# Performance work log

Hardware: AMD Instinct MI355X
Metric: run time of the kernel (lower is better)

## Reference

```python
import jax, jax.numpy as jnp
import numpy as np

B, T, D, R = 4, 2048, 1024, 32


def setup_inputs() -> dict:
    key = jax.random.key(0)
    kx, ku = jax.random.split(key)
    x = jax.random.normal(kx, (B, T, D), dtype=jnp.float32)
    # low-rank metric factor; small init so distances are moderate
    U = jax.random.normal(ku, (D, R), dtype=jnp.float32) * 0.05
    return {"x": x, "U": U}


def reference(x, U):
    # g = U @ U.T (PSD low-rank metric).
    # dist_sq[b,t,j] = (x_t - x_j)^T g (x_t - x_j)
    #               = ||U^T x_t||^2 + ||U^T x_j||^2 - 2 (U^T x_t).(U^T x_j)
    # Algebraic expansion of the original O(B*T*T*D) broadcasted diff tensor.
    y = jnp.einsum('btd,dr->btr', x, U)                # [B,T,R]
    n = jnp.sum(y * y, axis=-1)                         # [B,T]
    cross = jnp.einsum('btr,bjr->btj', y, y)            # [B,T,T]
    dist_sq = n[:, :, None] + n[:, None, :] - 2.0 * cross
    attn = jax.nn.softmax(-dist_sq, axis=-1)            # [B,T,T]
    return jnp.einsum('btj,bjd->btd', attn, x)          # [B,T,D]
```

## Files before the change

### kernel.cpp

```cpp
#include <hip/hip_runtime.h>

#define B_ 4
#define T_ 2048
#define D_ 1024
#define R_ 32
#define XSTR2 136
#define TT 64
#define TD 128
#define TJ 64
#define PSTR 72

typedef __attribute__((ext_vector_type(8))) short short8;
typedef __attribute__((ext_vector_type(4))) float f32x4;
typedef __attribute__((ext_vector_type(4))) unsigned short us4;
typedef __attribute__((ext_vector_type(8))) unsigned short us8;

__device__ __forceinline__ unsigned short f2bf(float f) {
  union { float f; unsigned u; } v; v.f = f;
  unsigned r = (v.u + 0x7fffu + ((v.u >> 16) & 1u)) >> 16;
  return (unsigned short)r;
}
__device__ __forceinline__ float bf2f(unsigned short h) {
  union { unsigned u; float f; } v; v.u = (unsigned)h << 16;
  return v.f;
}

__global__ __launch_bounds__(256)
void geo_ut(const float* __restrict__ U, unsigned short* __restrict__ Ut) {
  __shared__ float tile[128][33];
  const int tid = threadIdx.x;
  const int d0 = blockIdx.x * 128;
  #pragma unroll
  for (int i = 0; i < 16; i++) {
    int e = i * 256 + tid;
    int d = e >> 5, r = e & 31;
    tile[d][r] = U[(size_t)(d0 + d) * R_ + r];
  }
  __syncthreads();
  const int r = tid >> 3, seg = tid & 7;
  us8 o0, o1;
  #pragma unroll
  for (int k = 0; k < 8; k++) o0[k] = f2bf(tile[seg * 16 + k][r]);
  #pragma unroll
  for (int k = 0; k < 8; k++) o1[k] = f2bf(tile[seg * 16 + 8 + k][r]);
  *(us8*)(Ut + (size_t)r * D_ + d0 + seg * 16) = o0;
  *(us8*)(Ut + (size_t)r * D_ + d0 + seg * 16 + 8) = o1;
}

__global__ __launch_bounds__(256)
void geo_prep(const float* __restrict__ x, const unsigned short* __restrict__ Ut,
              unsigned short* __restrict__ xt, float* __restrict__ y_part) {
  __shared__ unsigned short xs[2][32 * XSTR2];
  const int b = blockIdx.y, slab = blockIdx.z;
  const int t0 = blockIdx.x * 32;
  const int d0 = slab * 256;
  const int tid = threadIdx.x, w = tid >> 6, lane = tid & 63;
  const int m = lane & 15, quad = lane >> 4;
  const int Mt = w & 1, Nt = w >> 1;
  const int lr = tid >> 3;
  const int lc = (tid & 7) * 16;

  const float* xb = x + ((size_t)b * T_ + t0 + lr) * D_ + d0 + lc;
  float4 v[2][4];
  #pragma unroll
  for (int ch = 0; ch < 2; ch++)
    #pragma unroll
    for (int i = 0; i < 4; i++)
      v[ch][i] = *(const float4*)(xb + ch * 128 + i * 4);
  #pragma unroll
  for (int ch = 0; ch < 2; ch++)
    #pragma unroll
    for (int i = 0; i < 4; i++) {
      us4 c;
      c[0] = f2bf(v[ch][i].x); c[1] = f2bf(v[ch][i].y);
      c[2] = f2bf(v[ch][i].z); c[3] = f2bf(v[ch][i].w);
      *(us4*)&xs[ch][lr * XSTR2 + lc + i * 4] = c;
    }
  __syncthreads();
  {
    const int wd = tid >> 1, wt = (tid & 1) * 16;
    #pragma unroll
    for (int ch = 0; ch < 2; ch++) {
      us8 o0, o1;
      #pragma unroll
      for (int k = 0; k < 8; k++) {
        o0[k] = xs[ch][(wt + k) * XSTR2 + wd];
        o1[k] = xs[ch][(wt + 8 + k) * XSTR2 + wd];
      }
      unsigned short* xo = xt + ((size_t)b * D_ + d0 + ch * 128 + wd) * T_ + t0;
      *(us8*)(xo + wt) = o0;
      *(us8*)(xo + wt + 8) = o1;
    }
  }
  f32x4 acc = {0.f, 0.f, 0.f, 0.f};
  #pragma unroll
  for (int ch = 0; ch < 2; ch++)
    #pragma unroll
    for (int ks = 0; ks < 4; ks++) {
      short8 af = *(const short8*)&xs[ch][(Mt * 16 + m) * XSTR2 + ks * 32 + quad * 8];
      short8 bf = *(const short8*)(Ut + (size_t)(Nt * 16 + m) * D_ + d0 + ch * 128 + ks * 32 + quad * 8);
      acc = __builtin_amdgcn_mfma_f32_16x16x32_bf16(af, bf, acc, 0, 0, 0);
    }
  float* yp = y_part + ((size_t)(slab * B_ + b) * T_ + t0 + Mt * 16 + quad * 4) * R_ + Nt * 16 + m;
  #pragma unroll
  for (int k = 0; k < 4; k++) yp[(size_t)k * R_] = acc[k];
}

__global__ __launch_bounds__(256)
void geo_reduce(const float* __restrict__ y_part, unsigned short* __restrict__ ybf,
                float* __restrict__ nsq) {
  const int tid = threadIdx.x;
  const size_t row = (size_t)blockIdx.x * 32 + (tid >> 3);
  const int r0 = (tid & 7) * 4;
  f32x4 v = {0.f, 0.f, 0.f, 0.f};
  #pragma unroll
  for (int s = 0; s < 4; s++) {
    f32x4 p = *(const f32x4*)(y_part + ((size_t)s * B_ * T_ + row) * R_ + r0);
    #pragma unroll
    for (int k = 0; k < 4; k++) v[k] += p[k];
  }
  us4 pk;
  float part = 0.f;
  #pragma unroll
  for (int k = 0; k < 4; k++) {
    pk[k] = f2bf(1.41421356237f * v[k]);
    float b = bf2f(pk[k]);
    part += b * b;
  }
  *(us4*)(ybf + row * R_ + r0) = pk;
  part += __shfl_xor(part, 1, 64);
  part += __shfl_xor(part, 2, 64);
  part += __shfl_xor(part, 4, 64);
  if ((tid & 7) == 0) nsq[row] = 0.5f * part;
}

__global__ __launch_bounds__(256)
void geo_fused(const unsigned short* __restrict__ ybf,
               const float* __restrict__ nsq,
               const unsigned short* __restrict__ xt,
               float* __restrict__ out) {
  __shared__ unsigned short XtS[TD * TJ];
  __shared__ unsigned short Pbuf[TT * PSTR];
  __shared__ float lred[4][TT];
  const int b = blockIdx.z;
  const int dt = blockIdx.x & 7, tt = blockIdx.x >> 3;
  const int t0 = tt * TT, d0 = dt * TD;
  const int tid = threadIdx.x, w = tid >> 6, lane = tid & 63;
  const int m = lane & 15, quad = lane >> 4;
  const int srow = lane >> 3, sslot = lane & 7;
  const unsigned short* yb = ybf + (size_t)b * T_ * R_;
  const float* nb = nsq + (size_t)b * T_;
  const unsigned short* xtb = xt + ((size_t)b * D_ + d0) * T_;

  short8 aq[4]; f32x4 ntv[4];
  #pragma unroll
  for (int s = 0; s < 4; s++) {
    aq[s]  = *(const short8*)(yb + (size_t)(t0 + s * 16 + m) * R_ + quad * 8);
    ntv[s] = *(const f32x4*)(nb + t0 + s * 16 + quad * 4);
  }
  f32x4 acc[4][2];
  f32x4 lsum[4];
  #pragma unroll
  for (int s = 0; s < 4; s++) {
    lsum[s] = (f32x4){0.f, 0.f, 0.f, 0.f};
    acc[s][0] = (f32x4){0.f, 0.f, 0.f, 0.f};
    acc[s][1] = (f32x4){0.f, 0.f, 0.f, 0.f};
  }

  for (int j0 = 0; j0 < T_; j0 += TJ) {
    if (j0) __syncthreads();
    #pragma unroll
    for (int cc = 0; cc < 4; cc++) {
      const int rd = w * 32 + cc * 8 + srow;
      const int gs = sslot ^ (rd & 7);
      __builtin_amdgcn_global_load_lds(
          (const __attribute__((address_space(1))) void*)(xtb + (size_t)rd * T_ + j0 + gs * 8),
          (__attribute__((address_space(3))) void*)(XtS + (w * 32 + cc * 8) * 64),
          16, 0, 0);
    }
    short8 bj = *(const short8*)(yb + (size_t)(j0 + w * 16 + m) * R_ + quad * 8);
    float nj = nb[j0 + w * 16 + m];
    #pragma unroll
    for (int s = 0; s < 4; s++) {
      f32x4 z = {0.f, 0.f, 0.f, 0.f};
      f32x4 c = __builtin_amdgcn_mfma_f32_16x16x32_bf16(aq[s], bj, z, 0, 0, 0);
      #pragma unroll
      for (int r = 0; r < 4; r++) {
        float p = __expf(c[r] - nj - ntv[s][r]);
        lsum[s][r] += p;
        Pbuf[(s * 16 + quad * 4 + r) * PSTR + w * 16 + m] = f2bf(p);
      }
    }
    __syncthreads();
    short8 bx[2][2];
    #pragma unroll
    for (int nt = 0; nt < 2; nt++) {
      const int dloc = w * 32 + nt * 16 + m;
      #pragma unroll
      for (int ks = 0; ks < 2; ks++)
        bx[nt][ks] = *(const short8*)(XtS + dloc * 64 + (((ks * 4 + quad) ^ (m & 7)) * 8));
    }
    #pragma unroll
    for (int s = 0; s < 4; s++) {
      short8 a0 = *(const short8*)(Pbuf + (s * 16 + m) * PSTR + quad * 8);
      short8 a1 = *(const short8*)(Pbuf + (s * 16 + m) * PSTR + 32 + quad * 8);
      #pragma unroll
      for (int nt = 0; nt < 2; nt++) {
        acc[s][nt] = __builtin_amdgcn_mfma_f32_16x16x32_bf16(a0, bx[nt][0], acc[s][nt], 0, 0, 0);
        acc[s][nt] = __builtin_amdgcn_mfma_f32_16x16x32_bf16(a1, bx[nt][1], acc[s][nt], 0, 0, 0);
      }
    }
  }
  #pragma unroll
  for (int s = 0; s < 4; s++)
    #pragma unroll
    for (int r = 0; r < 4; r++) {
      float v = lsum[s][r];
      v += __shfl_xor(v, 1, 64);
      v += __shfl_xor(v, 2, 64);
      v += __shfl_xor(v, 4, 64);
      v += __shfl_xor(v, 8, 64);
      lsum[s][r] = v;
    }
  if (m == 0) {
    #pragma unroll
    for (int s = 0; s < 4; s++)
      *(f32x4*)&lred[w][s * 16 + quad * 4] = lsum[s];
  }
  __syncthreads();
  float* ob = out + ((size_t)b * T_ + t0) * D_ + d0;
  #pragma unroll
  for (int s = 0; s < 4; s++) {
    f32x4 lt = *(const f32x4*)&lred[0][s * 16 + quad * 4];
    #pragma unroll
    for (int ww = 1; ww < 4; ww++) {
      f32x4 lv = *(const f32x4*)&lred[ww][s * 16 + quad * 4];
      #pragma unroll
      for (int r = 0; r < 4; r++) lt[r] += lv[r];
    }
    f32x4 inv;
    #pragma unroll
    for (int r = 0; r < 4; r++) inv[r] = 1.f / lt[r];
    #pragma unroll
    for (int nt = 0; nt < 2; nt++)
      #pragma unroll
      for (int r = 0; r < 4; r++)
        ob[(size_t)(s * 16 + quad * 4 + r) * D_ + w * 32 + nt * 16 + m] =
            acc[s][nt][r] * inv[r];
  }
}

extern "C" void kernel_launch(void* const* d_in, const int* in_sizes, int n_in,
                              void* d_out, int out_size, void* d_ws, size_t ws_size,
                              hipStream_t stream) {
  const float* x = (const float*)d_in[0];
  const float* U = (const float*)d_in[1];
  float* out = (float*)d_out;

  const size_t xt_b  = (size_t)B_ * D_ * T_ * 2;
  const size_t ybf_b = (size_t)B_ * T_ * R_ * 2;
  const size_t nsq_b = (size_t)B_ * T_ * 4;
  const size_t ut_b  = (size_t)D_ * R_ * 2;
  const size_t yp_b  = (size_t)4 * B_ * T_ * R_ * 4;

  char* wp = (char*)d_ws;
  unsigned short* xtp = (unsigned short*)wp;           wp += xt_b;
  unsigned short* ybf = (unsigned short*)wp;           wp += ybf_b;
  float* nsq = (float*)wp;                             wp += nsq_b;
  unsigned short* Utp = (unsigned short*)wp;           wp += ut_b;
  float* ypart = (float*)wp;                           wp += yp_b;
  (void)ws_size;

  hipLaunchKernelGGL(geo_ut, dim3(D_ / 128), dim3(256), 0, stream, U, Utp);
  hipLaunchKernelGGL(geo_prep, dim3(T_ / 32, B_, 4), dim3(256), 0, stream,
                     x, Utp, xtp, ypart);
  hipLaunchKernelGGL(geo_reduce, dim3(B_ * T_ / 32), dim3(256), 0, stream,
                     ypart, ybf, nsq);
  hipLaunchKernelGGL(geo_fused, dim3((T_ / TT) * (D_ / TD), 1, B_), dim3(256), 0, stream,
                     ybf, nsq, xtp, out);
}
```

Baseline: 181.8 us.

## Widen D tile to 256, use exp2 with folded log2e, transpose score MFMA

The feature tile per block doubles from 128 to 256 columns. The distance MFMA and the exponentials for each (t, j) tile are therefore computed half as often across the D dimension, and each wave now accumulates four 16-column output sub-tiles. The log2(e) factor is folded into the y scaling so the softmax can use exp2 directly. The score MFMA operands are swapped so each lane writes a contiguous us4 into the probability buffer and the row sum needs fewer shuffles. In exchange the grid has half as many blocks per batch and more accumulator registers are live, which may hurt occupancy. The launch-grid size must also match the new tile mapping, and that code is not shown.

New measurement: 158.6 us. 12.8% less time.

```diff
diff --git a/kernel.cpp b/kernel.cpp
--- a/kernel.cpp
+++ b/kernel.cpp
@@ -6,9 +6,10 @@
 #define R_ 32
 #define XSTR2 136
 #define TT 64
-#define TD 128
+#define TD 256
 #define TJ 64
 #define PSTR 72
+#define S2L 1.6986436f
 
 typedef __attribute__((ext_vector_type(8))) short short8;
 typedef __attribute__((ext_vector_type(4))) float f32x4;
@@ -123,7 +124,7 @@
   float part = 0.f;
   #pragma unroll
   for (int k = 0; k < 4; k++) {
-    pk[k] = f2bf(1.41421356237f * v[k]);
+    pk[k] = f2bf(S2L * v[k]);
     float b = bf2f(pk[k]);
     part += b * b;
   }
@@ -143,7 +144,7 @@
   __shared__ unsigned short Pbuf[TT * PSTR];
   __shared__ float lred[4][TT];
   const int b = blockIdx.z;
-  const int dt = blockIdx.x & 7, tt = blockIdx.x >> 3;
+  const int dt = blockIdx.x & 3, tt = blockIdx.x >> 2;
   const int t0 = tt * TT, d0 = dt * TD;
   const int tid = threadIdx.x, w = tid >> 6, lane = tid & 63;
   const int m = lane & 15, quad = lane >> 4;
@@ -152,80 +153,78 @@
   const float* nb = nsq + (size_t)b * T_;
   const unsigned short* xtb = xt + ((size_t)b * D_ + d0) * T_;
 
-  short8 aq[4]; f32x4 ntv[4];
-  #pragma unroll
-  for (int s = 0; s < 4; s++) {
-    aq[s]  = *(const short8*)(yb + (size_t)(t0 + s * 16 + m) * R_ + quad * 8);
-    ntv[s] = *(const f32x4*)(nb + t0 + s * 16 + quad * 4);
-  }
-  f32x4 acc[4][2];
-  f32x4 lsum[4];
-  #pragma unroll
-  for (int s = 0; s < 4; s++) {
-    lsum[s] = (f32x4){0.f, 0.f, 0.f, 0.f};
-    acc[s][0] = (f32x4){0.f, 0.f, 0.f, 0.f};
-    acc[s][1] = (f32x4){0.f, 0.f, 0.f, 0.f};
-  }
+  short8 bt[4]; float ntv[4];
+  #pragma unroll
+  for (int s = 0; s < 4; s++) {
+    bt[s]  = *(const short8*)(yb + (size_t)(t0 + s * 16 + m) * R_ + quad * 8);
+    ntv[s] = nb[t0 + s * 16 + m];
+  }
+  f32x4 acc[4][4];
+  float lsum[4] = {0.f, 0.f, 0.f, 0.f};
+  #pragma unroll
+  for (int s = 0; s < 4; s++)
+    #pragma unroll
+    for (int nt = 0; nt < 4; nt++)
+      acc[s][nt] = (f32x4){0.f, 0.f, 0.f, 0.f};
 
   for (int j0 = 0; j0 < T_; j0 += TJ) {
     if (j0) __syncthreads();
     #pragma unroll
-    for (int cc = 0; cc < 4; cc++) {
-      const int rd = w * 32 + cc * 8 + srow;
+    for (int cc = 0; cc < 8; cc++) {
+      const int rd = w * 64 + cc * 8 + srow;
       const int gs = sslot ^ (rd & 7);
       __builtin_amdgcn_global_load_lds(
           (const __attribute__((address_space(1))) void*)(xtb + (size_t)rd * T_ + j0 + gs * 8),
-          (__attribute__((address_space(3))) void*)(XtS + (w * 32 + cc * 8) * 64),
+          (__attribute__((address_space(3))) void*)(XtS + (w * 64 + cc * 8) * 64),
           16, 0, 0);
     }
-    short8 bj = *(const short8*)(yb + (size_t)(j0 + w * 16 + m) * R_ + quad * 8);
-    float nj = nb[j0 + w * 16 + m];
+    short8 aj = *(const short8*)(yb + (size_t)(j0 + w * 16 + m) * R_ + quad * 8);
+    f32x4 njv = *(const f32x4*)(nb + j0 + w * 16 + quad * 4);
     #pragma unroll
     for (int s = 0; s < 4; s++) {
       f32x4 z = {0.f, 0.f, 0.f, 0.f};
-      f32x4 c = __builtin_amdgcn_mfma_f32_16x16x32_bf16(aq[s], bj, z, 0, 0, 0);
+      f32x4 c = __builtin_amdgcn_mfma_f32_16x16x32_bf16(aj, bt[s], z, 0, 0, 0);
+      us4 pk;
+      float ls = 0.f;
       #pragma unroll
       for (int r = 0; r < 4; r++) {
-        float p = __expf(c[r] - nj - ntv[s][r]);
-        lsum[s][r] += p;
-        Pbuf[(s * 16 + quad * 4 + r) * PSTR + w * 16 + m] = f2bf(p);
+        float p = __builtin_exp2f(c[r] - njv[r] - ntv[s]);
+        ls += p;
+        pk[r] = f2bf(p);
       }
+      lsum[s] += ls;
+      *(us4*)(Pbuf + (s * 16 + m) * PSTR + w * 16 + quad * 4) = pk;
     }
     __syncthreads();
-    short8 bx[2][2];
-    #pragma unroll
-    for (int nt = 0; nt < 2; nt++) {
-      const int dloc = w * 32 + nt * 16 + m;
+    short8 bx[4][2];
+    #pragma unroll
+    for (int nt = 0; nt < 4; nt++) {
+      const int dloc = w * 64 + nt * 16 + m;
       #pragma unroll
       for (int ks = 0; ks < 2; ks++)
-        bx[nt][ks] = *(const short8*)(XtS + dloc * 64 + (((ks * 4 + quad) ^ (m & 7)) * 8));
+        bx[nt][ks] = *(const short8*)(XtS + dloc * 64 + (((ks * 4 + quad) ^ (dloc & 7)) * 8));
     }
     #pragma unroll
     for (int s = 0; s < 4; s++) {
       short8 a0 = *(const short8*)(Pbuf + (s * 16 + m) * PSTR + quad * 8);
       short8 a1 = *(const short8*)(Pbuf + (s * 16 + m) * PSTR + 32 + quad * 8);
       #pragma unroll
-      for (int nt = 0; nt < 2; nt++) {
+      for (int nt = 0; nt < 4; nt++) {
         acc[s][nt] = __builtin_amdgcn_mfma_f32_16x16x32_bf16(a0, bx[nt][0], acc[s][nt], 0, 0, 0);
         acc[s][nt] = __builtin_amdgcn_mfma_f32_16x16x32_bf16(a1, bx[nt][1], acc[s][nt], 0, 0, 0);
       }
     }
   }
   #pragma unroll
-  for (int s = 0; s < 4; s++)
-    #pragma unroll
-    for (int r = 0; r < 4; r++) {
-      float v = lsum[s][r];
-      v += __shfl_xor(v, 1, 64);
-      v += __shfl_xor(v, 2, 64);
-      v += __shfl_xor(v, 4, 64);
-      v += __shfl_xor(v, 8, 64);
-      lsum[s][r] = v;
-    }
-  if (m == 0) {
-    #pragma unroll
-    for (int s = 0; s < 4; s++)
-      *(f32x4*)&lred[w][s * 16 + quad * 4] = lsum[s];
+  for (int s = 0; s < 4; s++) {
+    float v = lsum[s];
+    v += __shfl_xor(v, 16, 64);
+    v += __shfl_xor(v, 32, 64);
+    lsum[s] = v;
+  }
+  if (quad == 0) {
+    #pragma unroll
+    for (int s = 0; s < 4; s++) lred[w][s * 16 + m] = lsum[s];
   }
   __syncthreads();
   float* ob = out + ((size_t)b * T_ + t0) * D_ + d0;
@@ -242,10 +241,10 @@
     #pragma unroll
     for (int r = 0; r < 4; r++) inv[r] = 1.f / lt[r];
     #pragma unroll
-    for (int nt = 0; nt < 2; nt++)
+    for (int nt = 0; nt < 4; nt++)
       #pragma unroll
       for (int r = 0; r < 4; r++)
-        ob[(size_t)(s * 16 + quad * 4 + r) * D_ + w * 32 + nt * 16 + m] =
+        ob[(size_t)(s * 16 + quad * 4 + r) * D_ + w * 64 + nt * 16 + m] =
             acc[s][nt][r] * inv[r];
   }
 }
```
